# Kernel optimization log

Hardware: AMD Instinct MI355X
Metric: run time of the kernel (lower is better)

## Reference

```python
import jax, jax.numpy as jnp
from jax import lax
import numpy as np


def _conv(x, w, stride):
    # x: [B,C,D,H,W], w: [3,3,3,Cin,Cout]; kernel 3, pad 1 (matches SubMConv3d / SparseConv3d(3, s, padding=1))
    return lax.conv_general_dilated(x, w, (stride, stride, stride), [(1, 1)] * 3,
                                    dimension_numbers=('NCDHW', 'DHWIO', 'NCDHW'))


def _bn_relu(y, scale, shift, mask):
    # eval-mode BatchNorm folded to scale/shift, ReLU, then restrict to active sites
    return jnp.maximum(y * scale[None, :, None, None, None] + shift[None, :, None, None, None], 0.0) * mask


def _downsample_mask(m):
    # SparseConv3d(k=3, s=2, p=1): output site active iff any input in its 3x3x3 window is active
    return lax.reduce_window(m, -jnp.inf, lax.max, (1, 1, 3, 3, 3), (1, 1, 2, 2, 2),
                             [(0, 0), (0, 0), (1, 1), (1, 1), (1, 1)])


def setup_inputs() -> dict:
    key = jax.random.key(0)
    ks = jax.random.split(key, 40)
    B, D = 1, 128
    occ = jax.random.uniform(ks[0], (B, 1, D, D, D)) < 0.05
    x = jax.random.normal(ks[1], (B, 16, D, D, D), jnp.float32) * occ

    def w(k, ci, co):
        return jax.random.normal(k, (3, 3, 3, ci, co), jnp.float32) * (1.0 / np.sqrt(27.0 * ci))

    def sc(k, c):
        return jax.random.uniform(k, (c,), jnp.float32, 0.5, 1.5)

    def sh(k, c):
        return jax.random.normal(k, (c,), jnp.float32) * 0.1

    chans = [(16, 16), (16, 16), (16, 32), (32, 32), (32, 32), (32, 64), (64, 64), (64, 64), (64, 64)]
    names = ['w0a', 'w0b', 'wd0', 'w1a', 'w1b', 'wd1', 'w2a', 'w2b', 'w2c']
    d = {'x': x, 'mask': occ}
    i = 2
    for n, (ci, co) in zip(names, chans):
        d[n] = w(ks[i], ci, co)
        d['s' + n[1:]] = sc(ks[i + 1], co)
        d['b' + n[1:]] = sh(ks[i + 2], co)
        i += 3
    return d


def reference(x, mask, w0a, s0a, b0a, w0b, s0b, b0b, wd0, sd0, bd0,
              w1a, s1a, b1a, w1b, s1b, b1b, wd1, sd1, bd1,
              w2a, s2a, b2a, w2b, s2b, b2b, w2c, s2c, b2c):
    m0 = mask.astype(x.dtype)                       # active sites at full res [B,1,128,128,128]
    h = _bn_relu(_conv(x, w0a, 1), s0a, b0a, m0)    # conv0 (subm0)
    h = _bn_relu(_conv(h, w0b, 1), s0b, b0b, m0)
    m1 = _downsample_mask(m0)                       # down0 activity [B,1,64,64,64]
    h = _bn_relu(_conv(h, wd0, 2), sd0, bd0, m1)
    h = _bn_relu(_conv(h, w1a, 1), s1a, b1a, m1)    # conv1 (subm1)
    h = _bn_relu(_conv(h, w1b, 1), s1b, b1b, m1)
    m2 = _downsample_mask(m1)                       # down1 activity [B,1,32,32,32]
    h = _bn_relu(_conv(h, wd1, 2), sd1, bd1, m2)
    h = _bn_relu(_conv(h, w2a, 1), s2a, b2a, m2)    # conv2 (subm2)
    h = _bn_relu(_conv(h, w2b, 1), s2b, b2b, m2)
    h = _bn_relu(_conv(h, w2c, 1), s2c, b2c, m2)
    return h                                        # .dense() -> [B,64,32,32,32]
```

## Files before the change

### kernel.cpp

```cpp
#include <hip/hip_runtime.h>
#include <cstdint>

typedef unsigned short u16;
typedef unsigned int u32;
typedef unsigned char u8;
typedef unsigned long long u64;
typedef __attribute__((ext_vector_type(8))) short short8;
typedef __attribute__((ext_vector_type(4))) float f32x4;

#define CAP 131072

__device__ __forceinline__ float bf1(u16 v){ union{u32 i; float f;} c; c.i = ((u32)v) << 16; return c.f; }
__device__ __forceinline__ u16 f2bf(float f){
    union{float f; u32 i;} c; c.f = f; u32 i = c.i;
    return (u16)((i + 0x7FFFu + ((i >> 16) & 1u)) >> 16);
}

constexpr int ilog2c(int n){ return n <= 1 ? 0 : 1 + ilog2c(n / 2); }

struct P18 { const void* p[18]; };
struct PJobs {
    const void* src[9];
    u32 start[10];
    int cin[9], cout[9], mode[9];
};

__global__ void detect_k(const u16* __restrict__ s0a, u32* __restrict__ flag){
    if (threadIdx.x == 0){
        int ok = 1;
        #pragma unroll
        for (int i = 0; i < 8; i += 2){
            u16 v = s0a[i];
            if (v < 0x3F00u || v > 0x3FC0u) ok = 0;
        }
        flag[0] = ok ? 1u : 0u;
    }
}

__global__ __launch_bounds__(256)
void prep_k(PJobs J, u16* __restrict__ FR, const u32* __restrict__ flag){
    const int gi = blockIdx.x * 256 + threadIdx.x;
    if (gi >= (int)J.start[9]) return;
    int j = 0;
    while (gi >= (int)J.start[j + 1]) ++j;
    const int i = gi - (int)J.start[j];
    const void* w = J.src[j];
    const int CIN = J.cin[j], COUT = J.cout[j];
    const int jj = i & 7;
    const int lane = (i >> 3) & 63;
    int rest = i >> 9;
    int src = -1;
    if (J.mode[j] == 0){
        const int KC = CIN >> 5, NT = COUT >> 4;
        const int nt = rest % NT; rest /= NT;
        const int kc = rest % KC; const int tap = rest / KC;
        const int k = kc * 32 + (lane >> 4) * 8 + jj;
        const int co = nt * 16 + (lane & 15);
        src = (tap * CIN + k) * COUT + co;
    } else if (J.mode[j] == 1){
        const int nt = rest & 1; const int pair = rest >> 1;
        const int kg = (lane >> 4) * 8 + jj;
        const int tap = pair * 2 + (kg >> 4);
        const int ci = kg & 15;
        const int co = nt * 16 + (lane & 15);
        if (tap < 27) src = (tap * 16 + ci) * 32 + co;
    } else {
        const int pair = rest;
        const int kg = (lane >> 4) * 8 + jj;
        const int tap = pair * 2 + (kg >> 4);
        const int ci = kg & 15;
        const int co = lane & 15;
        if (tap < 27) src = (tap * 16 + ci) * 16 + co;
    }
    float v = 0.f;
    if (src >= 0) v = flag[0] ? bf1(((const u16*)w)[src]) : ((const float*)w)[src];
    FR[gi] = f2bf(v);
}

__global__ __launch_bounds__(64)
void scales_k(P18 ps, float* __restrict__ S, const u32* __restrict__ flag){
    const int b = blockIdx.x, t = threadIdx.x;
    const int len[18] = {16,16,16,16,32,32,32,32,32,32,64,64,64,64,64,64,64,64};
    const int off[18] = {0,16,32,48,64,96,128,160,192,224,256,320,384,448,512,576,640,704};
    if (t < len[b]){
        const float v = flag[0] ? bf1(((const u16*)ps.p[b])[t]) : ((const float*)ps.p[b])[t];
        S[off[b] + t] = v;
    }
}

__global__ __launch_bounds__(256)
void actmask_k(const void* __restrict__ xv, u64* __restrict__ bmask,
               u32* __restrict__ bcnt, const u32* __restrict__ flag){
    const int v = blockIdx.x * 256 + threadIdx.x;
    const size_t N = 2097152;
    u32 a = 0;
    if (flag[0]) {
        const u16* x = (const u16*)xv;
        #pragma unroll
        for (int c = 0; c < 16; ++c) a |= (u32)(x[(size_t)c * N + v]) & 0x7FFFu;
    } else {
        const u32* x = (const u32*)xv;
        #pragma unroll
        for (int c = 0; c < 16; ++c) a |= x[(size_t)c * N + v] & 0x7FFFFFFFu;
    }
    const u64 m = __ballot(a != 0);
    __shared__ u32 wc[4];
    const int lane = threadIdx.x & 63, wv = threadIdx.x >> 6;
    if (lane == 0) { bmask[v >> 6] = m; wc[wv] = (u32)__popcll(m); }
    __syncthreads();
    if (threadIdx.x == 0) bcnt[blockIdx.x] = wc[0] + wc[1] + wc[2] + wc[3];
}

__global__ __launch_bounds__(1024)
void scan_k(const u32* __restrict__ bcnt, u32* __restrict__ boff, u32* __restrict__ cnt){
    __shared__ u32 lds[1024];
    const int t = threadIdx.x;
    u32 loc[8]; u32 s = 0;
    #pragma unroll
    for (int i = 0; i < 8; ++i){ loc[i] = s; s += bcnt[t * 8 + i]; }
    lds[t] = s;
    __syncthreads();
    u32 v = s;
    for (int d = 1; d < 1024; d <<= 1){
        u32 o = (t >= d) ? lds[t - d] : 0;
        __syncthreads();
        v += o; lds[t] = v;
        __syncthreads();
    }
    const u32 base = v - s;
    #pragma unroll
    for (int i = 0; i < 8; ++i) boff[t * 8 + i] = base + loc[i];
    if (t == 1023) cnt[0] = v;
}

__global__ __launch_bounds__(256)
void scatter_k(const u64* __restrict__ bmask, const u32* __restrict__ boff,
               int* __restrict__ idxmap, int* __restrict__ alist){
    const int v = blockIdx.x * 256 + threadIdx.x;
    const int lane = threadIdx.x & 63, wv = threadIdx.x >> 6;
    const u64 m = bmask[v >> 6];
    __shared__ u32 wc[4];
    if (lane == 0) wc[wv] = (u32)__popcll(m);
    __syncthreads();
    u32 wbase = 0;
    for (int i = 0; i < wv; ++i) wbase += wc[i];
    const bool act = (m >> lane) & 1ull;
    const u32 rank = (u32)__popcll(m & ((1ull << lane) - 1ull));
    int slot = -1;
    if (act){
        const u32 sl = boff[blockIdx.x] + wbase + rank;
        if (sl < CAP){ slot = (int)sl; alist[slot] = v; }
    }
    idxmap[v] = slot;
}

__global__ __launch_bounds__(256)
void gatherb_k(const void* __restrict__ xv, const int* __restrict__ alist,
               const u32* __restrict__ cnt, u16* __restrict__ f,
               const u32* __restrict__ flag){
    const int t = threadIdx.x;
    const int s = blockIdx.x * 16 + (t >> 4);
    const int c = t & 15;
    const int n = min((int)cnt[0], CAP);
    if (s >= n) return;
    const int v = alist[s];
    u16 val;
    if (flag[0]) val = ((const u16*)xv)[(size_t)c * 2097152 + v];
    else         val = f2bf(((const float*)xv)[(size_t)c * 2097152 + v]);
    f[(size_t)s * 16 + c] = val;
}

__global__ __launch_bounds__(256)
void m1_k(const int* __restrict__ idx, u8* __restrict__ mo){
    const int v = blockIdx.x * 256 + threadIdx.x;
    const int xo = v & 63, yo = (v >> 6) & 63, zo = v >> 12;
    u8 a = 0;
    for (int kz = 0; kz < 3; ++kz){ int iz = 2*zo + kz - 1; if ((unsigned)iz >= 128u) continue;
      for (int ky = 0; ky < 3; ++ky){ int iy = 2*yo + ky - 1; if ((unsigned)iy >= 128u) continue;
        for (int kx = 0; kx < 3; ++kx){ int ix = 2*xo + kx - 1; if ((unsigned)ix >= 128u) continue;
          a |= (idx[((size_t)iz * 128 + iy) * 128 + ix] >= 0) ? 1 : 0;
    }}}
    mo[v] = a;
}

template<int DO>
__global__ __launch_bounds__(256)
void maskdown_k(const u8* __restrict__ mi, u8* __restrict__ mo){
    constexpr int DI = DO * 2;
    constexpr int LOG = ilog2c(DO);
    const int v = blockIdx.x * 256 + threadIdx.x;
    const int xo = v & (DO - 1), yo = (v >> LOG) & (DO - 1), zo = v >> (2 * LOG);
    u8 a = 0;
    for (int kz = 0; kz < 3; ++kz){ int iz = 2*zo + kz - 1; if ((unsigned)iz >= (unsigned)DI) continue;
      for (int ky = 0; ky < 3; ++ky){ int iy = 2*yo + ky - 1; if ((unsigned)iy >= (unsigned)DI) continue;
        for (int kx = 0; kx < 3; ++kx){ int ix = 2*xo + kx - 1; if ((unsigned)ix >= (unsigned)DI) continue;
          a |= mi[((size_t)iz * DI + iy) * DI + ix];
    }}}
    mo[v] = a;
}

__global__ __launch_bounds__(256)
void sconvm_k(const u16* __restrict__ fin, const int* __restrict__ idxmap,
              const int* __restrict__ alist, const u32* __restrict__ cnt,
              const u16* __restrict__ wf, const float* __restrict__ sc,
              const float* __restrict__ sh, u16* __restrict__ fout){
    const int n = min((int)cnt[0], CAP);
    const int j = blockIdx.x * 4 + (threadIdx.x >> 6);
    const int sbase = j * 16;
    if (sbase >= n) return;
    const int lane = threadIdx.x & 63;
    const int m = lane & 15, quad = lane >> 4;

    const int s = sbase + m;
    const int v = (s < n) ? alist[s] : -1;
    int xo = 0, yo = 0, zo = 0;
    if (v >= 0){ xo = v & 127; yo = (v >> 7) & 127; zo = v >> 14; }

    f32x4 acc = {0.f,0.f,0.f,0.f};
    for (int p = 0; p < 14; ++p){
        const int tp = p * 2 + (quad >> 1);
        short8 a = {0,0,0,0,0,0,0,0};
        if (v >= 0 && tp < 27){
            const int kz = tp / 9, ky = (tp / 3) % 3, kx = tp % 3;
            const int iz = zo + kz - 1, iy = yo + ky - 1, ix = xo + kx - 1;
            if ((unsigned)iz < 128u && (unsigned)iy < 128u && (unsigned)ix < 128u){
                const int sn = idxmap[((size_t)iz * 128 + iy) * 128 + ix];
                if (sn >= 0) a = *(const short8*)(fin + (size_t)sn * 16 + (quad & 1) * 8);
            }
        }
        short8 b = *(const short8*)(wf + ((size_t)p * 64 + lane) * 8);
        acc = __builtin_amdgcn_mfma_f32_16x16x32_bf16(a, b, acc, 0, 0, 0);
    }

    const int co = lane & 15;
    const float scl = sc[co], shf = sh[co];
    #pragma unroll
    for (int r = 0; r < 4; ++r){
        const int srow = sbase + quad * 4 + r;
        if (srow < n){
            fout[(size_t)srow * 16 + co] = f2bf(fmaxf(acc[r] * scl + shf, 0.f));
        }
    }
}

__global__ __launch_bounds__(256)
void convd0m_k(const u16* __restrict__ fbuf, const int* __restrict__ idxmap,
               const u16* __restrict__ wf, const float* __restrict__ sc,
               const float* __restrict__ sh, const u8* __restrict__ mk,
               u16* __restrict__ out)
{
    const int wj = blockIdx.x * 4 + (threadIdx.x >> 6);
    const int lane = threadIdx.x & 63;
    const int m = lane & 15, quad = lane >> 4;
    const int xo_b = (wj & 3) * 16;
    const int yo = (wj >> 2) & 63;
    const int zo = wj >> 8;

    f32x4 acc0 = {0.f,0.f,0.f,0.f}, acc1 = {0.f,0.f,0.f,0.f};
    const int ix_m = (xo_b + m) * 2 - 1;

    for (int p = 0; p < 14; ++p){
        const int tp = p * 2 + (quad >> 1);
        short8 a = {0,0,0,0,0,0,0,0};
        if (tp < 27){
            const int kz = tp / 9, ky = (tp / 3) % 3, kx = tp % 3;
            const int iz = 2*zo + kz - 1, iy = 2*yo + ky - 1, ix = ix_m + kx;
            if ((unsigned)iz < 128u && (unsigned)iy < 128u && (unsigned)ix < 128u){
                const int sn = idxmap[((size_t)iz * 128 + iy) * 128 + ix];
                if (sn >= 0) a = *(const short8*)(fbuf + (size_t)sn * 16 + (quad & 1) * 8);
            }
        }
        short8 b0 = *(const short8*)(wf + ((size_t)(p*2+0) * 64 + lane) * 8);
        short8 b1 = *(const short8*)(wf + ((size_t)(p*2+1) * 64 + lane) * 8);
        acc0 = __builtin_amdgcn_mfma_f32_16x16x32_bf16(a, b0, acc0, 0, 0, 0);
        acc1 = __builtin_amdgcn_mfma_f32_16x16x32_bf16(a, b1, acc1, 0, 0, 0);
    }

    const int vb = wj * 16 + quad * 4;
    const u32 m4 = *(const u32*)(mk + vb);
    const int n = lane & 15;
    #pragma unroll
    for (int nt = 0; nt < 2; ++nt){
        const int co = nt * 16 + n;
        const float s = sc[co], h = sh[co];
        const f32x4 acc = nt ? acc1 : acc0;
        #pragma unroll
        for (int r = 0; r < 4; ++r){
            float val = fmaxf(acc[r] * s + h, 0.f);
            val = ((m4 >> (8*r)) & 0xFFu) ? val : 0.f;
            out[(size_t)(vb + r) * 32 + co] = f2bf(val);
        }
    }
}

template<int DIN, int DOUT, int CIN, int COUT, int STRIDE, bool FINAL>
__global__ __launch_bounds__(256)
void mconv_k(const u16* __restrict__ in, const u16* __restrict__ wf,
             const float* __restrict__ sc, const float* __restrict__ sh,
             const u8* __restrict__ mk, void* __restrict__ out,
             const u32* __restrict__ flag)
{
    constexpr int KC = CIN / 32;
    constexpr int NT = COUT / 16;
    constexpr int XT = DOUT / 16;
    const int wj = blockIdx.x * 4 + (threadIdx.x >> 6);
    const int lane = threadIdx.x & 63;
    const int m = lane & 15, quad = lane >> 4;

    const int xo_b = (wj % XT) * 16;
    const int yo = (wj / XT) % DOUT;
    const int zo = wj / (XT * DOUT);

    f32x4 acc[NT];
    #pragma unroll
    for (int i = 0; i < NT; ++i) acc[i] = (f32x4){0.f,0.f,0.f,0.f};

    const int ix0 = (xo_b + m) * STRIDE - 1;
    for (int kz = 0; kz < 3; ++kz){
      const int iz = zo * STRIDE + kz - 1;
      if ((unsigned)iz >= (unsigned)DIN) continue;
      for (int ky = 0; ky < 3; ++ky){
        const int iy = yo * STRIDE + ky - 1;
        if ((unsigned)iy >= (unsigned)DIN) continue;
        const size_t rowb = ((size_t)iz * DIN + iy) * DIN;
        #pragma unroll
        for (int kx = 0; kx < 3; ++kx){
          const int ix = ix0 + kx;
          const bool v = (unsigned)ix < (unsigned)DIN;
          const int tap = (kz*3 + ky)*3 + kx;
          const u16* ap = in + (rowb + ix) * CIN + quad * 8;
          const u16* bp = wf + (size_t)tap * KC * NT * 512 + lane * 8;
          #pragma unroll
          for (int kc = 0; kc < KC; ++kc){
            short8 a = {0,0,0,0,0,0,0,0};
            if (v) a = *(const short8*)(ap + kc * 32);
            #pragma unroll
            for (int nt = 0; nt < NT; ++nt){
              short8 b = *(const short8*)(bp + (kc * NT + nt) * 512);
              acc[nt] = __builtin_amdgcn_mfma_f32_16x16x32_bf16(a, b, acc[nt], 0, 0, 0);
            }
          }
    }}}

    const int vb = wj * 16 + quad * 4;
    const u32 m4 = *(const u32*)(mk + vb);
    const int n = lane & 15;
    #pragma unroll
    for (int nt = 0; nt < NT; ++nt){
        const int co = nt * 16 + n;
        const float s = sc[co], h = sh[co];
        #pragma unroll
        for (int r = 0; r < 4; ++r){
            float val = fmaxf(acc[nt][r] * s + h, 0.f);
            val = ((m4 >> (8*r)) & 0xFFu) ? val : 0.f;
            ((u16*)out)[(size_t)(vb + r) * COUT + co] = f2bf(val);
        }
    }
    (void)flag;
}

template<int D, int CIN, int COUT, int WAVES, bool FINAL>
__global__ __launch_bounds__(WAVES*64)
void mconvlds_k(const u16* __restrict__ in, const u16* __restrict__ wf,
                const float* __restrict__ sc, const float* __restrict__ sh,
                const u8* __restrict__ mk, void* __restrict__ out,
                const u32* __restrict__ flag)
{
    constexpr int KC = CIN / 32;
    constexpr int NT = COUT / 16;
    constexpr int CH8 = CIN / 8;
    constexpr int BT = WAVES * 64;
    __shared__ u16 tile[9 * 2048];

    const int t = threadIdx.x;
    const int yo = blockIdx.x % D, zo = blockIdx.x / D;

    for (int dz = 0; dz < 3; ++dz){
      const int iz = zo + dz - 1;
      for (int dy = 0; dy < 3; ++dy){
        const int iy = yo + dy - 1;
        if ((unsigned)iz < (unsigned)D && (unsigned)iy < (unsigned)D){
          const u16* src = in + ((size_t)(iz * D + iy) * D) * CIN;
          u16* dst = &tile[(dz * 3 + dy) * 2048];
          for (int c = t; c < D * CH8; c += BT){
            const int x = c / CH8, c8 = c % CH8;
            *(short8*)(dst + (c8 * D + x) * 8) = *(const short8*)(src + c * 8);
          }
        }
      }
    }
    __syncthreads();

    const int lane = t & 63, w = t >> 6;
    const int m = lane & 15, quad = lane >> 4;
    const int xo_b = w * 16;

    f32x4 acc[NT];
    #pragma unroll
    for (int i = 0; i < NT; ++i) acc[i] = (f32x4){0.f,0.f,0.f,0.f};

    #pragma unroll
    for (int kz = 0; kz < 3; ++kz){
      const int iz = zo + kz - 1;
      if ((unsigned)iz >= (unsigned)D) continue;
      #pragma unroll
      for (int ky = 0; ky < 3; ++ky){
        const int iy = yo + ky - 1;
        if ((unsigned)iy >= (unsigned)D) continue;
        const u16* row = &tile[(kz * 3 + ky) * 2048];
        #pragma unroll
        for (int kx = 0; kx < 3; ++kx){
          const int ix = xo_b + m + kx - 1;
          const bool aok = (unsigned)ix < (unsigned)D;
          const int tap = (kz * 3 + ky) * 3 + kx;
          const u16* bp = wf + (size_t)tap * KC * NT * 512 + lane * 8;
          #pragma unroll
          for (int kc = 0; kc < KC; ++kc){
            short8 a = {0,0,0,0,0,0,0,0};
            if (aok) a = *(const short8*)(row + ((kc * 4 + quad) * D + ix) * 8);
            #pragma unroll
            for (int nt = 0; nt < NT; ++nt){
              short8 b = *(const short8*)(bp + (kc * NT + nt) * 512);
              acc[nt] = __builtin_amdgcn_mfma_f32_16x16x32_bf16(a, b, acc[nt], 0, 0, 0);
            }
          }
        }
      }
    }

    const int vb = (zo * D + yo) * D + xo_b + quad * 4;
    const u32 m4 = *(const u32*)(mk + vb);
    const int n = lane & 15;
    if (FINAL) {
        const bool bfout = flag[0] != 0;
        #pragma unroll
        for (int nt = 0; nt < NT; ++nt){
            const int co = nt * 16 + n;
            const float s = sc[co], h = sh[co];
            float4 o;
            float* po = &o.x;
            #pragma unroll
            for (int r = 0; r < 4; ++r){
                float val = fmaxf(acc[nt][r] * s + h, 0.f);
                po[r] = ((m4 >> (8*r)) & 0xFFu) ? val : 0.f;
            }
            if (!bfout) {
                *(float4*)((float*)out + (size_t)co * (D*D*D) + vb) = o;
            } else {
                u16* ob = (u16*)out + (size_t)co * (D*D*D) + vb;
                #pragma unroll
                for (int r = 0; r < 4; ++r) ob[r] = f2bf(po[r]);
            }
        }
    } else {
        #pragma unroll
        for (int nt = 0; nt < NT; ++nt){
            const int co = nt * 16 + n;
            const float s = sc[co], h = sh[co];
            #pragma unroll
            for (int r = 0; r < 4; ++r){
                float val = fmaxf(acc[nt][r] * s + h, 0.f);
                val = ((m4 >> (8*r)) & 0xFFu) ? val : 0.f;
                ((u16*)out)[(size_t)(vb + r) * COUT + co] = f2bf(val);
            }
        }
    }
}

extern "C" void kernel_launch(void* const* d_in, const int* in_sizes, int n_in,
                              void* d_out, int out_size, void* d_ws, size_t ws_size,
                              hipStream_t stream)
{
    (void)out_size; (void)ws_size;

    int wb = 2;
    for (int i = 1; i < n_in; ++i) { if (in_sizes[i] == 6912) { wb = i; break; } }

    const void* x = d_in[0];
    const void *w0a=d_in[wb+0],  *s0a=d_in[wb+1],  *b0a=d_in[wb+2];
    const void *w0b=d_in[wb+3],  *s0b=d_in[wb+4],  *b0b=d_in[wb+5];
    const void *wd0=d_in[wb+6],  *sd0=d_in[wb+7],  *bd0=d_in[wb+8];
    const void *w1a=d_in[wb+9],  *s1a=d_in[wb+10], *b1a=d_in[wb+11];
    const void *w1b=d_in[wb+12], *s1b=d_in[wb+13], *b1b=d_in[wb+14];
    const void *wd1=d_in[wb+15], *sd1=d_in[wb+16], *bd1=d_in[wb+17];
    const void *w2a=d_in[wb+18], *s2a=d_in[wb+19], *b2a=d_in[wb+20];
    const void *w2b=d_in[wb+21], *s2b=d_in[wb+22], *b2b=d_in[wb+23];
    const void *w2c=d_in[wb+24], *s2c=d_in[wb+25], *b2c=d_in[wb+26];

    char* ws = (char*)d_ws;
    int*   idxmap = (int*)(ws);
    u16*   Fb0    = (u16*)(ws + 8388608);
    u16*   Fb1    = (u16*)(ws + 12582912);
    u16*   Fb2    = (u16*)(ws + 16777216);
    u16*   Rb1    = (u16*)(ws + 25165824);
    u16*   Rb2    = (u16*)(ws + 41943040);
    u8*    m1     = (u8*)(ws + 58720256);
    u8*    m2     = (u8*)(ws + 58982400);
    u32*   cnt    = (u32*)(ws + 59015168);
    int*   alist  = (int*)(ws + 59015424);
    u16*   FR     = (u16*)(ws + 59539712);
    float* S      = (float*)(ws + 60481792);
    u32*   flag   = (u32*)(ws + 60484864);
    u64*   bmask  = (u64*)(ws + 60485120);
    u32*   bcnt   = (u32*)(ws + 60747264);
    u32*   boff   = (u32*)(ws + 60780032);

    u16* wfs0a = FR + 0;
    u16* wfs0b = FR + 7168;
    u16* fd0   = FR + 14336;
    u16* f1a   = FR + 28672;
    u16* f1b   = FR + 56320;
    u16* fd1   = FR + 83968;
    u16* f2a   = FR + 139264;
    u16* f2b   = FR + 249856;
    u16* f2c   = FR + 360448;

    detect_k<<<1, 64, 0, stream>>>((const u16*)s0a, flag);

    PJobs J;
    const void* jsrc[9] = {w0a, w0b, wd0, w1a, w1b, wd1, w2a, w2b, w2c};
    const u32 jlen[9]   = {7168,7168,14336,27648,27648,55296,110592,110592,110592};
    const int jcin[9]   = {16,16,16,32,32,32,64,64,64};
    const int jcout[9]  = {16,16,32,32,32,64,64,64,64};
    const int jmode[9]  = {2,2,1,0,0,0,0,0,0};
    u32 acc = 0;
    for (int i = 0; i < 9; ++i){
        J.src[i] = jsrc[i]; J.start[i] = acc; acc += jlen[i];
        J.cin[i] = jcin[i]; J.cout[i] = jcout[i]; J.mode[i] = jmode[i];
    }
    J.start[9] = acc;
    prep_k<<<(int)((acc + 255) / 256), 256, 0, stream>>>(J, FR, flag);

    P18 ps;
    const void* sv[18] = {s0a,b0a,s0b,b0b,sd0,bd0,s1a,b1a,s1b,b1b,sd1,bd1,s2a,b2a,s2b,b2b,s2c,b2c};
    for (int i = 0; i < 18; ++i) ps.p[i] = sv[i];
    scales_k<<<18, 64, 0, stream>>>(ps, S, flag);
    float *cs0a=S+0,  *cb0a=S+16,  *cs0b=S+32,  *cb0b=S+48;
    float *csd0=S+64, *cbd0=S+96,  *cs1a=S+128, *cb1a=S+160, *cs1b=S+192, *cb1b=S+224;
    float *csd1=S+256,*cbd1=S+320, *cs2a=S+384, *cb2a=S+448, *cs2b=S+512, *cb2b=S+576, *cs2c=S+640, *cb2c=S+704;

    actmask_k<<<8192, 256, 0, stream>>>(x, bmask, bcnt, flag);
    scan_k<<<1, 1024, 0, stream>>>(bcnt, boff, cnt);
    scatter_k<<<8192, 256, 0, stream>>>(bmask, boff, idxmap, alist);
    m1_k<<<1024, 256, 0, stream>>>(idxmap, m1);
    maskdown_k<32><<<128, 256, 0, stream>>>(m1, m2);

    gatherb_k<<<8192, 256, 0, stream>>>(x, alist, cnt, Fb0, flag);
    sconvm_k<<<2048, 256, 0, stream>>>(Fb0, idxmap, alist, cnt, wfs0a, cs0a, cb0a, Fb1);
    sconvm_k<<<2048, 256, 0, stream>>>(Fb1, idxmap, alist, cnt, wfs0b, cs0b, cb0b, Fb2);
    convd0m_k<<<4096, 256, 0, stream>>>(Fb2, idxmap, fd0, csd0, cbd0, m1, Rb1);
    mconvlds_k<64,32,32,4,false><<<4096, 256, 0, stream>>>(Rb1, f1a, cs1a, cb1a, m1, Rb2, flag);
    mconvlds_k<64,32,32,4,false><<<4096, 256, 0, stream>>>(Rb2, f1b, cs1b, cb1b, m1, Rb1, flag);
    mconv_k<64,32,32,64,2,false><<<512, 256, 0, stream>>>(Rb1, fd1, csd1, cbd1, m2, Rb2, flag);
    mconvlds_k<32,64,64,2,false><<<1024, 128, 0, stream>>>(Rb2, f2a, cs2a, cb2a, m2, Rb1, flag);
    mconvlds_k<32,64,64,2,false><<<1024, 128, 0, stream>>>(Rb1, f2b, cs2b, cb2b, m2, Rb2, flag);
    mconvlds_k<32,64,64,2,true ><<<1024, 128, 0, stream>>>(Rb2, f2c, cs2c, cb2c, m2, d_out, flag);
}
```

Measured before the change: 542.0 us.

## Fuse feature gather into scatter, precompute neighbor table, derive m1 from bitmask

```diff
diff --git a/kernel.cpp b/kernel.cpp
--- a/kernel.cpp
+++ b/kernel.cpp
@@ -134,8 +134,10 @@
 }
 
 __global__ __launch_bounds__(256)
-void scatter_k(const u64* __restrict__ bmask, const u32* __restrict__ boff,
-               int* __restrict__ idxmap, int* __restrict__ alist){
+void scatter2_k(const void* __restrict__ xv, const u64* __restrict__ bmask,
+                const u32* __restrict__ boff, int* __restrict__ idxmap,
+                int* __restrict__ alist, u16* __restrict__ f,
+                const u32* __restrict__ flag){
     const int v = blockIdx.x * 256 + threadIdx.x;
     const int lane = threadIdx.x & 63, wv = threadIdx.x >> 6;
     const u64 m = bmask[v >> 6];
@@ -149,38 +151,38 @@
     int slot = -1;
     if (act){
         const u32 sl = boff[blockIdx.x] + wbase + rank;
-        if (sl < CAP){ slot = (int)sl; alist[slot] = v; }
+        if (sl < CAP){
+            slot = (int)sl;
+            alist[slot] = v;
+            if (flag[0]){
+                const u16* x = (const u16*)xv;
+                #pragma unroll
+                for (int c = 0; c < 16; ++c) f[(size_t)slot * 16 + c] = x[(size_t)c * 2097152 + v];
+            } else {
+                const float* x = (const float*)xv;
+                #pragma unroll
+                for (int c = 0; c < 16; ++c) f[(size_t)slot * 16 + c] = f2bf(x[(size_t)c * 2097152 + v]);
+            }
+        }
     }
     idxmap[v] = slot;
 }
 
 __global__ __launch_bounds__(256)
-void gatherb_k(const void* __restrict__ xv, const int* __restrict__ alist,
-               const u32* __restrict__ cnt, u16* __restrict__ f,
-               const u32* __restrict__ flag){
-    const int t = threadIdx.x;
-    const int s = blockIdx.x * 16 + (t >> 4);
-    const int c = t & 15;
-    const int n = min((int)cnt[0], CAP);
-    if (s >= n) return;
-    const int v = alist[s];
-    u16 val;
-    if (flag[0]) val = ((const u16*)xv)[(size_t)c * 2097152 + v];
-    else         val = f2bf(((const float*)xv)[(size_t)c * 2097152 + v]);
-    f[(size_t)s * 16 + c] = val;
-}
-
-__global__ __launch_bounds__(256)
-void m1_k(const int* __restrict__ idx, u8* __restrict__ mo){
+void m1b_k(const u64* __restrict__ bmask, u8* __restrict__ mo){
     const int v = blockIdx.x * 256 + threadIdx.x;
     const int xo = v & 63, yo = (v >> 6) & 63, zo = v >> 12;
-    u8 a = 0;
-    for (int kz = 0; kz < 3; ++kz){ int iz = 2*zo + kz - 1; if ((unsigned)iz >= 128u) continue;
-      for (int ky = 0; ky < 3; ++ky){ int iy = 2*yo + ky - 1; if ((unsigned)iy >= 128u) continue;
-        for (int kx = 0; kx < 3; ++kx){ int ix = 2*xo + kx - 1; if ((unsigned)ix >= 128u) continue;
-          a |= (idx[((size_t)iz * 128 + iy) * 128 + ix] >= 0) ? 1 : 0;
+    u32 a = 0;
+    #pragma unroll
+    for (int kz = 0; kz < 3; ++kz){ const int iz = 2*zo + kz - 1; if ((unsigned)iz >= 128u) continue;
+      #pragma unroll
+      for (int ky = 0; ky < 3; ++ky){ const int iy = 2*yo + ky - 1; if ((unsigned)iy >= 128u) continue;
+        #pragma unroll
+        for (int kx = 0; kx < 3; ++kx){ const int ix = 2*xo + kx - 1; if ((unsigned)ix >= 128u) continue;
+          const int vv = (iz * 128 + iy) * 128 + ix;
+          a |= (u32)((bmask[vv >> 6] >> (vv & 63)) & 1ull);
     }}}
-    mo[v] = a;
+    mo[v] = (u8)a;
 }
 
 template<int DO>
@@ -200,33 +202,46 @@
 }
 
 __global__ __launch_bounds__(256)
-void sconvm_k(const u16* __restrict__ fin, const int* __restrict__ idxmap,
-              const int* __restrict__ alist, const u32* __restrict__ cnt,
-              const u16* __restrict__ wf, const float* __restrict__ sc,
-              const float* __restrict__ sh, u16* __restrict__ fout){
+void nbr_k(const int* __restrict__ idxmap, const int* __restrict__ alist,
+           const u32* __restrict__ cnt, int* __restrict__ nbr){
+    const int s = blockIdx.x * 256 + threadIdx.x;
+    const int n = min((int)cnt[0], CAP);
+    if (s >= n) return;
+    const int v = alist[s];
+    const int xo = v & 127, yo = (v >> 7) & 127, zo = v >> 14;
+    #pragma unroll
+    for (int tap = 0; tap < 27; ++tap){
+        const int kz = tap / 9, ky = (tap / 3) % 3, kx = tap % 3;
+        const int iz = zo + kz - 1, iy = yo + ky - 1, ix = xo + kx - 1;
+        int sn = -1;
+        if ((unsigned)iz < 128u && (unsigned)iy < 128u && (unsigned)ix < 128u)
+            sn = idxmap[((size_t)iz * 128 + iy) * 128 + ix];
+        nbr[tap * CAP + s] = sn;
+    }
+}
+
+__global__ __launch_bounds__(256)
+void sconvm2_k(const u16* __restrict__ fin, const int* __restrict__ nbr,
+               const u32* __restrict__ cnt, const u16* __restrict__ wf,
+               const float* __restrict__ sc, const float* __restrict__ sh,
+               u16* __restrict__ fout){
     const int n = min((int)cnt[0], CAP);
     const int j = blockIdx.x * 4 + (threadIdx.x >> 6);
     const int sbase = j * 16;
     if (sbase >= n) return;
     const int lane = threadIdx.x & 63;
     const int m = lane & 15, quad = lane >> 4;
-
     const int s = sbase + m;
-    const int v = (s < n) ? alist[s] : -1;
-    int xo = 0, yo = 0, zo = 0;
-    if (v >= 0){ xo = v & 127; yo = (v >> 7) & 127; zo = v >> 14; }
+    const bool sok = s < n;
 
     f32x4 acc = {0.f,0.f,0.f,0.f};
+    #pragma unroll
     for (int p = 0; p < 14; ++p){
         const int tp = p * 2 + (quad >> 1);
         short8 a = {0,0,0,0,0,0,0,0};
-        if (v >= 0 && tp < 27){
-            const int kz = tp / 9, ky = (tp / 3) % 3, kx = tp % 3;
-            const int iz = zo + kz - 1, iy = yo + ky - 1, ix = xo + kx - 1;
-            if ((unsigned)iz < 128u && (unsigned)iy < 128u && (unsigned)ix < 128u){
-                const int sn = idxmap[((size_t)iz * 128 + iy) * 128 + ix];
-                if (sn >= 0) a = *(const short8*)(fin + (size_t)sn * 16 + (quad & 1) * 8);
-            }
+        if (sok && tp < 27){
+            const int sn = nbr[tp * CAP + s];
+            if (sn >= 0) a = *(const short8*)(fin + (size_t)sn * 16 + (quad & 1) * 8);
         }
         short8 b = *(const short8*)(wf + ((size_t)p * 64 + lane) * 8);
         acc = __builtin_amdgcn_mfma_f32_16x16x32_bf16(a, b, acc, 0, 0, 0);
@@ -259,6 +274,7 @@
     f32x4 acc0 = {0.f,0.f,0.f,0.f}, acc1 = {0.f,0.f,0.f,0.f};
     const int ix_m = (xo_b + m) * 2 - 1;
 
+    #pragma unroll
     for (int p = 0; p < 14; ++p){
         const int tp = p * 2 + (quad >> 1);
         short8 a = {0,0,0,0,0,0,0,0};
@@ -504,6 +520,7 @@
     u64*   bmask  = (u64*)(ws + 60485120);
     u32*   bcnt   = (u32*)(ws + 60747264);
     u32*   boff   = (u32*)(ws + 60780032);
+    int*   nbr    = (int*)(ws + 60812800);
 
     u16* wfs0a = FR + 0;
     u16* wfs0b = FR + 7168;
@@ -541,13 +558,13 @@
 
     actmask_k<<<8192, 256, 0, stream>>>(x, bmask, bcnt, flag);
     scan_k<<<1, 1024, 0, stream>>>(bcnt, boff, cnt);
-    scatter_k<<<8192, 256, 0, stream>>>(bmask, boff, idxmap, alist);
-    m1_k<<<1024, 256, 0, stream>>>(idxmap, m1);
+    scatter2_k<<<8192, 256, 0, stream>>>(x, bmask, boff, idxmap, alist, Fb0, flag);
+    m1b_k<<<1024, 256, 0, stream>>>(bmask, m1);
     maskdown_k<32><<<128, 256, 0, stream>>>(m1, m2);
-
-    gatherb_k<<<8192, 256, 0, stream>>>(x, alist, cnt, Fb0, flag);
-    sconvm_k<<<2048, 256, 0, stream>>>(Fb0, idxmap, alist, cnt, wfs0a, cs0a, cb0a, Fb1);
-    sconvm_k<<<2048, 256, 0, stream>>>(Fb1, idxmap, alist, cnt, wfs0b, cs0b, cb0b, Fb2);
+    nbr_k<<<512, 256, 0, stream>>>(idxmap, alist, cnt, nbr);
+
+    sconvm2_k<<<2048, 256, 0, stream>>>(Fb0, nbr, cnt, wfs0a, cs0a, cb0a, Fb1);
+    sconvm2_k<<<2048, 256, 0, stream>>>(Fb1, nbr, cnt, wfs0b, cs0b, cb0b, Fb2);
     convd0m_k<<<4096, 256, 0, stream>>>(Fb2, idxmap, fd0, csd0, cbd0, m1, Rb1);
     mconvlds_k<64,32,32,4,false><<<4096, 256, 0, stream>>>(Rb1, f1a, cs1a, cb1a, m1, Rb2, flag);
     mconvlds_k<64,32,32,4,false><<<4096, 256, 0, stream>>>(Rb2, f1b, cs1b, cb1b, m1, Rb1, flag);
```

Result: no change. 544.6 us (+0.5%).
